# Optimization experiments

Hardware: AMD Instinct MI355X
Metric: run time of the kernel (lower is better)

## Reference

```python
import jax, jax.numpy as jnp
import numpy as np

B, C, H = 4, 1, 256          # batch, channels, square image size
A, P = 180, 256              # n_angles, n_detector_positions
T = int(np.ceil(np.sqrt(2.0) * H))  # samples per ray (covers image diagonal) = 363


def setup_inputs() -> dict:
    key = jax.random.key(0)
    x = jax.random.normal(key, (B, C, H, H), dtype=jnp.float32)
    # projection angles uniformly covering [0, pi)
    thetas = (jnp.pi * jnp.arange(A, dtype=jnp.float32) / A)
    # detector offsets in pixel units, centered on the image center
    positions = jnp.arange(P, dtype=jnp.float32) - (P - 1) / 2.0
    return {"x": x, "thetas": thetas, "positions": positions}


def _radon(x, thetas, positions):
    """Radon transform: line integrals along rays (theta, s) with bilinear
    sampling at unit spacing along each ray. Returns sinogram [B,C,A,P]."""
    Bc, Cc, Hh, Ww = x.shape
    cx = (Ww - 1) / 2.0
    cy = (Hh - 1) / 2.0
    t = jnp.arange(T, dtype=x.dtype) - (T - 1) / 2.0          # [T] along-ray param
    cos = jnp.cos(thetas)[:, None, None]                       # [A,1,1]
    sin = jnp.sin(thetas)[:, None, None]
    s = positions[None, :, None]                               # [1,P,1]
    tt = t[None, None, :]                                      # [1,1,T]
    # rotated ray sample coordinates, [A,P,T]
    px = cx + s * cos - tt * sin
    py = cy + s * sin + tt * cos
    x0 = jnp.floor(px)
    y0 = jnp.floor(py)
    wx = px - x0
    wy = py - y0
    x0i = x0.astype(jnp.int32)
    y0i = y0.astype(jnp.int32)

    def gather(iy, ix):
        # zero outside the image (zero-padding boundary)
        valid = (ix >= 0) & (ix < Ww) & (iy >= 0) & (iy < Hh)
        ixc = jnp.clip(ix, 0, Ww - 1)
        iyc = jnp.clip(iy, 0, Hh - 1)
        v = x[:, :, iyc, ixc]                                  # [B,C,A,P,T]
        return v * valid.astype(x.dtype)

    interp = (gather(y0i,     x0i)     * ((1.0 - wx) * (1.0 - wy))
            + gather(y0i,     x0i + 1) * (wx * (1.0 - wy))
            + gather(y0i + 1, x0i)     * ((1.0 - wx) * wy)
            + gather(y0i + 1, x0i + 1) * (wx * wy))
    return interp.sum(axis=-1)                                 # [B,C,A,P]


def reference(x, thetas, positions):
    return _radon(x, thetas, positions)
```

## Files before the change

kernel.cpp:

```cpp
#include <hip/hip_runtime.h>
#include <hip/hip_fp16.h>


#define NB   4
#define NA   180
#define NP   256
#define GANG 3
#define NSEG 4

#define STRIDE_A 261
#define ROWS_A   135
#define STRIDE_B 138
#define ROWS_B   259
#define IMG_DW   (ROWS_B * STRIDE_B)
#define RED_OFF  (IMG_DW * 4)
#define SMEM_BYTES (RED_OFF + NP * NSEG * 4)

__device__ __forceinline__ unsigned pack_h2(float a, float b) {
    __half2 h = __halves2half2(__float2half_rn(a), __float2half_rn(b));
    return *reinterpret_cast<unsigned*>(&h);
}

template<int STRIDE>
__device__ __forceinline__ float ray_accum(
    const unsigned int* __restrict__ imgw,
    float bxr, float byr, float nsv, float cv,
    float xlo, float xhi, float ylo, float yhi,
    int tlo, int thi, int seg)
{
    float acc = 0.f;
    int   t  = tlo + seg;
    float pxu = fmaf((float)t - 181.0f, nsv, bxr);
    float pyu = fmaf((float)t - 181.0f, cv,  byr);
    const float dpx = 4.0f * nsv;
    const float dpy = 4.0f * cv;
    #pragma unroll 4
    for (; t < thi; t += 4) {
        float px = __builtin_amdgcn_fmed3f(pxu, xlo, xhi);
        float py = __builtin_amdgcn_fmed3f(pyu, ylo, yhi);
        pxu += dpx;
        pyu += dpy;
        const float fx = floorf(px);
        const float fy = floorf(py);
        const float wx = px - fx;
        const float wy = py - fy;
        const int ad = (int)fmaf(fy, (float)STRIDE, fx);
        const unsigned q0 = imgw[ad];
        const unsigned q1 = imgw[ad + 1];
        unsigned A = __builtin_amdgcn_perm(q1, q0, 0x05040100u);
        unsigned B = __builtin_amdgcn_perm(q1, q0, 0x07060302u);
        const __half2 hA = *reinterpret_cast<__half2*>(&A);
        const __half2 hB = *reinterpret_cast<__half2*>(&B);
        const __half2 wy2 = __half2half2(__float2half_rn(wy));
        const __half2 V = __hfma2(wy2, __hsub2(hB, hA), hA);
        const float vlo = __half2float(__low2half(V));
        const float vhi = __half2float(__high2half(V));
        acc = fmaf(wx, vhi - vlo, acc + vlo);
    }
    return acc;
}

extern "C" __global__ __launch_bounds__(1024)
void radon_fwd(const float* __restrict__ x,
               const float* __restrict__ thetas,
               const float* __restrict__ positions,
               float* __restrict__ out)
{
    extern __shared__ unsigned char smem[];
    unsigned int* imgw = (unsigned int*)smem;
    float*        red  = (float*)(smem + RED_OFF);

    const int grp  = blockIdx.x;
    const int b    = blockIdx.y;
    const int half = blockIdx.z;
    const int a0   = grp * GANG;
    const bool regA = (a0 < 45) || (a0 >= 135);
    const int tid = threadIdx.x + (threadIdx.y << 8);
    const float* __restrict__ xb = x + b * 65536;
    const float4* __restrict__ xb4 = (const float4*)xb;

    for (int i = tid; i < IMG_DW; i += 1024) imgw[i] = 0u;
    __syncthreads();

    if (regA) {
        const int Fb = half ? 122 : -2;
        for (int d = tid; d < ROWS_A * 64; d += 1024) {
            const int r  = d >> 6;
            const int j  = d & 63;
            const int R0 = Fb + r, R1 = R0 + 1;
            const int r0c = min(max(R0, 0), 255), r1c = min(max(R1, 0), 255);
            const float4 f0 = xb4[r0c * 64 + j];
            const float4 f1 = xb4[r1c * 64 + j];
            const bool m0 = ((unsigned)R0 < 256u), m1 = ((unsigned)R1 < 256u);
            const float t0x = m0 ? f0.x : 0.f, t0y = m0 ? f0.y : 0.f,
                        t0z = m0 ? f0.z : 0.f, t0w = m0 ? f0.w : 0.f;
            const float t1x = m1 ? f1.x : 0.f, t1y = m1 ? f1.y : 0.f,
                        t1z = m1 ? f1.z : 0.f, t1w = m1 ? f1.w : 0.f;
            const int cb = r * STRIDE_A + 4 * j + 2;
            imgw[cb + 0] = pack_h2(t0x, t1x);
            imgw[cb + 1] = pack_h2(t0y, t1y);
            imgw[cb + 2] = pack_h2(t0z, t1z);
            imgw[cb + 3] = pack_h2(t0w, t1w);
        }
    } else {
        for (int d = tid; d < ROWS_B * 34; d += 1024) {
            const int r = d / 34;
            const int j = d - r * 34;
            const int R0 = r - 2, R1 = r - 1;
            const int r0c = min(max(R0, 0), 255), r1c = min(max(R1, 0), 255);
            const int col4 = j + (half ? 30 : 0);
            const float4 f0 = xb4[r0c * 64 + col4];
            const float4 f1 = xb4[r1c * 64 + col4];
            const bool m0 = ((unsigned)R0 < 256u), m1 = ((unsigned)R1 < 256u);
            const float t0x = m0 ? f0.x : 0.f, t0y = m0 ? f0.y : 0.f,
                        t0z = m0 ? f0.z : 0.f, t0w = m0 ? f0.w : 0.f;
            const float t1x = m1 ? f1.x : 0.f, t1y = m1 ? f1.y : 0.f,
                        t1z = m1 ? f1.z : 0.f, t1w = m1 ? f1.w : 0.f;
            const int cb = r * STRIDE_B + 4 * j + (half ? 0 : 2);
            imgw[cb + 0] = pack_h2(t0x, t1x);
            imgw[cb + 1] = pack_h2(t0y, t1y);
            imgw[cb + 2] = pack_h2(t0z, t1z);
            imgw[cb + 3] = pack_h2(t0w, t1w);
        }
    }
    __syncthreads();

    float xlo, xhi, ylo, yhi, CbX, CbY;
    if (regA) {
        xlo = 0.f; xhi = 259.0f;
        ylo = 0.f; yhi = 134.984375f;
        CbX = -2.f; CbY = half ? 122.f : -2.f;
    } else {
        xlo = 0.f; xhi = 136.984375f;
        ylo = 0.f; yhi = 258.984375f;
        CbX = half ? 120.f : -2.f; CbY = -2.f;
    }

    const int   p   = threadIdx.x;
    const int   seg = threadIdx.y;
    const float s   = positions[p];

    float accs[GANG];
    for (int g = 0; g < GANG; ++g) {
        const float th  = thetas[a0 + g];
        const float cv  = cosf(th);
        const float sv  = sinf(th);
        const float nsv = -sv;
        const float bxI = fmaf(s, cv, 127.5f);
        const float byI = fmaf(s, sv, 127.5f);

        const float slope = regA ? cv : nsv;
        const float base  = regA ? byI : bxI;
        const float tstar = 181.0f + (128.0f - base) / slope;
        const float Sf    = (slope > 0.f) ? ceilf(tstar) : (floorf(tstar) + 1.0f);
        const int   S     = (int)fmaxf(0.f, fminf(364.f, Sf));
        const bool  h0Low = (slope > 0.f);
        const int lo = ((half == 0) == h0Low) ? 0 : S;
        const int hi = ((half == 0) == h0Low) ? S : 364;

        const float msx = (fabsf(sv) < 1e-7f) ? copysignf(1e-7f, sv) : sv;
        const float mcy = (fabsf(cv) < 1e-7f) ? copysignf(1e-7f, cv) : cv;
        const float invx = -1.0f / msx;
        const float invy =  1.0f / mcy;
        const float ux1 = (-2.0f  - bxI) * invx;
        const float ux2 = (257.0f - bxI) * invx;
        const float uy1 = (-2.0f  - byI) * invy;
        const float uy2 = (257.0f - byI) * invy;
        const float ulo = fmaxf(fminf(ux1, ux2), fminf(uy1, uy2));
        const float uhi = fminf(fmaxf(ux1, ux2), fmaxf(uy1, uy2));
        const float tbf = ceilf(ulo + 181.0f) - 1.0f;
        const float tef = floorf(uhi + 181.0f) + 2.0f;
        const int tb = (int)fmaxf((float)lo, fminf(364.0f, tbf));
        const int te = (int)fminf((float)hi, fmaxf(0.0f,  tef));

        const float bxr = bxI - CbX;
        const float byr = byI - CbY;
        accs[g] = regA
            ? ray_accum<STRIDE_A>(imgw, bxr, byr, nsv, cv, xlo, xhi, ylo, yhi, tb, te, seg)
            : ray_accum<STRIDE_B>(imgw, bxr, byr, nsv, cv, xlo, xhi, ylo, yhi, tb, te, seg);
    }

    for (int g = 0; g < GANG; ++g) {
        __syncthreads();
        red[(seg << 8) + p] = accs[g];
        __syncthreads();
        if (seg == 0) {
            float r4 = red[p] + red[256 + p] + red[512 + p] + red[768 + p];
            atomicAdd(&out[b * (NA * NP) + (a0 + g) * NP + p], r4);
        }
    }
}

extern "C" void kernel_launch(void* const* d_in, const int* in_sizes, int n_in,
                              void* d_out, int out_size, void* d_ws, size_t ws_size,
                              hipStream_t stream) {
    const float* x         = (const float*)d_in[0];
    const float* thetas    = (const float*)d_in[1];
    const float* positions = (const float*)d_in[2];
    float* out = (float*)d_out;

    hipFuncSetAttribute((const void*)radon_fwd,
                        hipFuncAttributeMaxDynamicSharedMemorySize, SMEM_BYTES);

    hipMemsetAsync(d_out, 0, (size_t)out_size * sizeof(float), stream);

    dim3 grid(NA / GANG, NB, 2);
    dim3 block(NP, NSEG);
    radon_fwd<<<grid, block, SMEM_BYTES, stream>>>(x, thetas, positions, out);
}
```

Before: 116.1 us.

## Fill shared image tile per-element, drop zero-init pass, widen unroll

The shared-memory image staging now writes every dword exactly once, with per-element bounds checks that emit zeros for padding. This removes the separate zero-fill pass and its barrier. The cost is scalar global loads in place of float4 loads, plus integer divisions by the stride. The region-B stride grows by one dword, likely to change LDS bank mapping, and the ray loop unroll rises from 4 to 8.

```diff
diff --git a/kernel.cpp b/kernel.cpp
--- a/kernel.cpp
+++ b/kernel.cpp
@@ -10,9 +10,11 @@
 
 #define STRIDE_A 261
 #define ROWS_A   135
-#define STRIDE_B 138
+#define STRIDE_B 139
 #define ROWS_B   259
-#define IMG_DW   (ROWS_B * STRIDE_B)
+#define DW_A     (ROWS_A * STRIDE_A)
+#define DW_B     (ROWS_B * STRIDE_B)
+#define IMG_DW   DW_B
 #define RED_OFF  (IMG_DW * 4)
 #define SMEM_BYTES (RED_OFF + NP * NSEG * 4)
 
@@ -34,7 +36,7 @@
     float pyu = fmaf((float)t - 181.0f, cv,  byr);
     const float dpx = 4.0f * nsv;
     const float dpy = 4.0f * cv;
-    #pragma unroll 4
+    #pragma unroll 8
     for (; t < thi; t += 4) {
         float px = __builtin_amdgcn_fmed3f(pxu, xlo, xhi);
         float py = __builtin_amdgcn_fmed3f(pyu, ylo, yhi);
@@ -77,50 +79,30 @@
     const bool regA = (a0 < 45) || (a0 >= 135);
     const int tid = threadIdx.x + (threadIdx.y << 8);
     const float* __restrict__ xb = x + b * 65536;
-    const float4* __restrict__ xb4 = (const float4*)xb;
-
-    for (int i = tid; i < IMG_DW; i += 1024) imgw[i] = 0u;
-    __syncthreads();
 
     if (regA) {
         const int Fb = half ? 122 : -2;
-        for (int d = tid; d < ROWS_A * 64; d += 1024) {
-            const int r  = d >> 6;
-            const int j  = d & 63;
+        for (int d = tid; d < DW_A; d += 1024) {
+            const int r  = d / STRIDE_A;
+            const int c  = d - r * STRIDE_A;
+            const int gc = c - 2;
             const int R0 = Fb + r, R1 = R0 + 1;
-            const int r0c = min(max(R0, 0), 255), r1c = min(max(R1, 0), 255);
-            const float4 f0 = xb4[r0c * 64 + j];
-            const float4 f1 = xb4[r1c * 64 + j];
-            const bool m0 = ((unsigned)R0 < 256u), m1 = ((unsigned)R1 < 256u);
-            const float t0x = m0 ? f0.x : 0.f, t0y = m0 ? f0.y : 0.f,
-                        t0z = m0 ? f0.z : 0.f, t0w = m0 ? f0.w : 0.f;
-            const float t1x = m1 ? f1.x : 0.f, t1y = m1 ? f1.y : 0.f,
-                        t1z = m1 ? f1.z : 0.f, t1w = m1 ? f1.w : 0.f;
-            const int cb = r * STRIDE_A + 4 * j + 2;
-            imgw[cb + 0] = pack_h2(t0x, t1x);
-            imgw[cb + 1] = pack_h2(t0y, t1y);
-            imgw[cb + 2] = pack_h2(t0z, t1z);
-            imgw[cb + 3] = pack_h2(t0w, t1w);
+            const bool gok = ((unsigned)gc < 256u);
+            const float v0 = (gok && (unsigned)R0 < 256u) ? xb[R0 * 256 + gc] : 0.f;
+            const float v1 = (gok && (unsigned)R1 < 256u) ? xb[R1 * 256 + gc] : 0.f;
+            imgw[d] = pack_h2(v0, v1);
         }
     } else {
-        for (int d = tid; d < ROWS_B * 34; d += 1024) {
-            const int r = d / 34;
-            const int j = d - r * 34;
+        const int cofs = half ? 120 : -2;
+        for (int d = tid; d < DW_B; d += 1024) {
+            const int r  = d / STRIDE_B;
+            const int c  = d - r * STRIDE_B;
+            const int gc = c + cofs;
             const int R0 = r - 2, R1 = r - 1;
-            const int r0c = min(max(R0, 0), 255), r1c = min(max(R1, 0), 255);
-            const int col4 = j + (half ? 30 : 0);
-            const float4 f0 = xb4[r0c * 64 + col4];
-            const float4 f1 = xb4[r1c * 64 + col4];
-            const bool m0 = ((unsigned)R0 < 256u), m1 = ((unsigned)R1 < 256u);
-            const float t0x = m0 ? f0.x : 0.f, t0y = m0 ? f0.y : 0.f,
-                        t0z = m0 ? f0.z : 0.f, t0w = m0 ? f0.w : 0.f;
-            const float t1x = m1 ? f1.x : 0.f, t1y = m1 ? f1.y : 0.f,
-                        t1z = m1 ? f1.z : 0.f, t1w = m1 ? f1.w : 0.f;
-            const int cb = r * STRIDE_B + 4 * j + (half ? 0 : 2);
-            imgw[cb + 0] = pack_h2(t0x, t1x);
-            imgw[cb + 1] = pack_h2(t0y, t1y);
-            imgw[cb + 2] = pack_h2(t0z, t1z);
-            imgw[cb + 3] = pack_h2(t0w, t1w);
+            const bool gok = ((unsigned)gc < 256u);
+            const float v0 = (gok && (unsigned)R0 < 256u) ? xb[R0 * 256 + gc] : 0.f;
+            const float v1 = (gok && (unsigned)R1 < 256u) ? xb[R1 * 256 + gc] : 0.f;
+            imgw[d] = pack_h2(v0, v1);
         }
     }
     __syncthreads();
```

Result: slower. 141.5 us (+22.0%).
